# Optimization experiments

Measured on AMD Instinct MI355X. Metric: run time of the kernel, lower is better.

The kernel has to match this reference:

```python
import jax, jax.numpy as jnp
import numpy as np

SUBNET_NUM = 32
BATCH = 131072
H1, H2 = 10, 6          # subnet_arch = [10, 6]
SMOOTH_LAMBDA = 0.001
BN_EPS = 1e-10


def setup_inputs() -> dict:
    key = jax.random.key(0)
    ks = jax.random.split(key, 7)
    f32 = jnp.float32
    x = jax.random.normal(ks[0], (BATCH, SUBNET_NUM), f32)
    # small init scale keeps tanh in its non-saturated (smooth) regime
    W1 = 0.5 * jax.random.normal(ks[1], (SUBNET_NUM, 1, H1), f32)
    b1 = 0.1 * jax.random.normal(ks[2], (SUBNET_NUM, H1), f32)
    W2 = 0.5 * jax.random.normal(ks[3], (SUBNET_NUM, H1, H2), f32)
    b2 = 0.1 * jax.random.normal(ks[4], (SUBNET_NUM, H2), f32)
    W3 = 0.5 * jax.random.normal(ks[5], (SUBNET_NUM, H2, 1), f32)
    b3 = 0.1 * jax.random.normal(ks[6], (SUBNET_NUM, 1), f32)
    return {"x": x, "W1": W1, "b1": b1, "W2": W2, "b2": b2, "W3": W3, "b3": b3}


def _subnet_scalar(x_s, w1, b1, w2, b2, w3, b3):
    """One subnet applied to one scalar input: output and d2out/dx2."""
    def f(xs):
        h = jnp.tanh(xs * w1[0] + b1)        # [H1]  (input dim is 1)
        h = jnp.tanh(h @ w2 + b2)            # [H2]
        return (h @ w3)[0] + b3[0]           # scalar
    out = f(x_s)
    g2 = jax.grad(jax.grad(f))(x_s)          # second derivative wrt the scalar input
    return out, g2


def reference(x, W1, b1, W2, b2, W3, b3):
    # vmap over batch (inner) and over subnets (outer, axis 1 of x / axis 0 of params)
    per_batch = jax.vmap(_subnet_scalar, in_axes=(0, None, None, None, None, None, None))
    per_subnet = jax.vmap(per_batch, in_axes=(1, 0, 0, 0, 0, 0, 0), out_axes=(1, 1))
    out, g2 = per_subnet(x, W1, b1, W2, b2, W3, b3)      # each [BATCH, SUBNET_NUM]

    # BatchNorm (momentum=0.0, center=False, scale=False) in training mode:
    # normalize by batch stats; moving_variance == biased batch variance.
    mean = jnp.mean(out, axis=0)
    var = jnp.mean((out - mean) ** 2, axis=0)
    out_bn = (out - mean) * jax.lax.rsqrt(var + BN_EPS)

    # smooth penalty per subnet: mean(grad2^2) / sqrt(moving_variance)
    penalty = jnp.mean(g2 ** 2, axis=0) / jnp.sqrt(var)
    smooth_loss = SMOOTH_LAMBDA * jnp.sum(penalty)
    return out_bn, smooth_loss
```

## Files before the change

kernel.cpp:

```cpp
#include <hip/hip_runtime.h>

#define BATCH 131072
#define SN 32
#define H1 10
#define H2 6
#define ROWS 128
#define GRID (BATCH / ROWS)
#define TPB 512
#define LDS_STRIDE 33

#define FB 512
#define FT 256

typedef float v2f __attribute__((ext_vector_type(2)));

__device__ __forceinline__ v2f bc(float s) { v2f r; r.x = s; r.y = s; return r; }
__device__ __forceinline__ v2f fma2(v2f a, v2f b, v2f c) {
    return __builtin_elementwise_fma(a, b, c);
}
__device__ __forceinline__ v2f tanh2(v2f x) {
    v2f x2 = x + x;
    v2f e; e.x = __expf(x2.x); e.y = __expf(x2.y);
    v2f e1 = e + bc(1.0f);
    v2f r; r.x = __builtin_amdgcn_rcpf(e1.x); r.y = __builtin_amdgcn_rcpf(e1.y);
    return fma2(bc(-2.0f), r, bc(1.0f));
}

__device__ __forceinline__ float wave_sum(float v) {
    v += __int_as_float(__builtin_amdgcn_update_dpp(
            0, __float_as_int(v), 0x111, 0xf, 0xf, false));
    v += __int_as_float(__builtin_amdgcn_update_dpp(
            0, __float_as_int(v), 0x112, 0xf, 0xf, false));
    v += __int_as_float(__builtin_amdgcn_update_dpp(
            0, __float_as_int(v), 0x114, 0xf, 0xf, false));
    v += __int_as_float(__builtin_amdgcn_update_dpp(
            0, __float_as_int(v), 0x118, 0xf, 0xf, false));
    v += __int_as_float(__builtin_amdgcn_update_dpp(
            0, __float_as_int(v), 0x142, 0xa, 0xf, false));
    v += __int_as_float(__builtin_amdgcn_update_dpp(
            0, __float_as_int(v), 0x143, 0xc, 0xf, false));
    return v;
}

__global__ __launch_bounds__(TPB) void k_main(
    const float* __restrict__ x,
    const float* __restrict__ W1, const float* __restrict__ B1,
    const float* __restrict__ W2, const float* __restrict__ B2,
    const float* __restrict__ W3, const float* __restrict__ B3,
    float* __restrict__ out, float* __restrict__ partial )
{
    __shared__ float xt[ROWS * LDS_STRIDE];
    const int tid = threadIdx.x;
    const int lane = tid & 63;
    const int wave = tid >> 6;
    const int blk = blockIdx.x;

    const float4* xv = (const float4*)(x + (size_t)blk * ROWS * SN);
    #pragma unroll
    for (int it = 0; it < 2; ++it) {
        int v = it * TPB + tid;
        float4 val = xv[v];
        int r = v >> 3;
        int c = (v & 7) << 2;
        float* dst = &xt[r * LDS_STRIDE + c];
        dst[0] = val.x; dst[1] = val.y; dst[2] = val.z; dst[3] = val.w;
    }
    __syncthreads();

    #pragma unroll 1
    for (int si = 0; si < 4; ++si) {
        const int s = __builtin_amdgcn_readfirstlane(si * 8 + wave);
        const float* w1p = W1 + s * H1;
        const float* b1p = B1 + s * H1;
        const float* w2p = W2 + s * H1 * H2;
        const float* b2p = B2 + s * H2;
        const float* w3p = W3 + s * H2;
        const float b3 = B3[s];

        float w1r[H1], b1r[H1];
        #pragma unroll
        for (int i = 0; i < H1; ++i) { w1r[i] = w1p[i]; b1r[i] = b1p[i]; }
        float w2r[H1 * H2];
        #pragma unroll
        for (int k = 0; k < H1 * H2; ++k) w2r[k] = w2p[k];
        float b2r[H2], w3r[H2];
        #pragma unroll
        for (int j = 0; j < H2; ++j) { b2r[j] = b2p[j]; w3r[j] = w3p[j]; }

        v2f xs;
        xs.x = xt[lane * LDS_STRIDE + s];
        xs.y = xt[(lane + 64) * LDS_STRIDE + s];

        v2f t[H1], p[H1], q[H1];
        #pragma unroll
        for (int i = 0; i < H1; ++i) {
            v2f u = fma2(xs, bc(w1r[i]), bc(b1r[i]));
            v2f ti = tanh2(u);
            v2f e = fma2(-ti, ti, bc(1.0f));
            t[i] = ti;
            p[i] = e * bc(w1r[i]);
            q[i] = (ti * p[i]) * bc(w1r[i]);
        }

        v2f o = bc(b3), g2a = bc(0.0f);
        #pragma unroll
        for (int j = 0; j < H2; ++j) {
            v2f vv = bc(b2r[j]), a = bc(0.0f), c = bc(0.0f);
            #pragma unroll
            for (int i = 0; i < H1; ++i) {
                v2f wb = bc(w2r[i * H2 + j]);
                vv = fma2(wb, t[i], vv);
                a  = fma2(wb, p[i], a);
                c  = fma2(wb, q[i], c);
            }
            v2f sj = tanh2(vv);
            v2f dj = fma2(-sj, sj, bc(1.0f));
            v2f aa = a * a;
            v2f h  = fma2(sj, aa, c);
            v2f k  = dj * h;
            o   = fma2(bc(w3r[j]), sj, o);
            g2a = fma2(bc(w3r[j]), k, g2a);
        }

        xt[lane * LDS_STRIDE + s] = o.x;
        xt[(lane + 64) * LDS_STRIDE + s] = o.y;

        v2f s2v = o * o;
        v2f s3v = (g2a * g2a) * bc(4.0f);
        float s1 = wave_sum(o.x + o.y);
        float s2 = wave_sum(s2v.x + s2v.y);
        float s3 = wave_sum(s3v.x + s3v.y);
        if (lane == 63) {
            partial[(size_t)(0 * SN + s) * GRID + blk] = s1;
            partial[(size_t)(1 * SN + s) * GRID + blk] = s2;
            partial[(size_t)(2 * SN + s) * GRID + blk] = s3;
        }
    }
    __syncthreads();

    float4* po = (float4*)out;
    const size_t base = (size_t)blk * (ROWS * SN / 4);
    #pragma unroll
    for (int it = 0; it < 2; ++it) {
        int v = it * TPB + tid;
        int r = v >> 3;
        int c = (v & 7) << 2;
        const float* src = &xt[r * LDS_STRIDE + c];
        float4 w; w.x = src[0]; w.y = src[1]; w.z = src[2]; w.w = src[3];
        po[base + v] = w;
    }
}

__global__ __launch_bounds__(FT) void k_finish(float* __restrict__ out,
                                               const float* __restrict__ partial)
{
    __shared__ double red_s[3 * SN];
    __shared__ float mean_s[SN], inv_s[SN];
    const int tid = threadIdx.x;
    const int lane = tid & 63;
    const int wave = tid >> 6;

    for (int r = wave; r < 3 * SN; r += 4) {
        const float4* pr = (const float4*)(partial + (size_t)r * GRID);
        double sd = 0.0;
        #pragma unroll
        for (int k = 0; k < 4; ++k) {
            float4 v4 = pr[k * 64 + lane];
            sd += (double)v4.x + (double)v4.y + (double)v4.z + (double)v4.w;
        }
        #pragma unroll
        for (int off = 32; off > 0; off >>= 1) sd += __shfl_down(sd, off);
        if (lane == 0) red_s[r] = sd;
    }
    __syncthreads();

    const double invB = 1.0 / (double)BATCH;
    if (tid < SN) {
        double mean = red_s[tid] * invB;
        double var = red_s[SN + tid] * invB - mean * mean;
        if (var < 0.0) var = 0.0;
        mean_s[tid] = (float)mean;
        inv_s[tid] = (float)(1.0 / sqrt(var + 1e-10));
    }
    if (blockIdx.x == 0 && tid == 0) {
        double sum = 0.0;
        for (int s = 0; s < SN; ++s) {
            double mean = red_s[s] * invB;
            double var = red_s[SN + s] * invB - mean * mean;
            if (var < 0.0) var = 0.0;
            sum += (red_s[2 * SN + s] * invB) / sqrt(var);
        }
        out[(size_t)BATCH * SN] = (float)(0.001 * sum);
    }
    __syncthreads();

    float4* p = (float4*)out;
    const int total = BATCH * SN / 4;
    for (int v = blockIdx.x * FT + tid; v < total; v += FB * FT) {
        float4 val = p[v];
        const int c = (v & 7) << 2;
        val.x = (val.x - mean_s[c + 0]) * inv_s[c + 0];
        val.y = (val.y - mean_s[c + 1]) * inv_s[c + 1];
        val.z = (val.z - mean_s[c + 2]) * inv_s[c + 2];
        val.w = (val.w - mean_s[c + 3]) * inv_s[c + 3];
        p[v] = val;
    }
}

extern "C" void kernel_launch(void* const* d_in, const int* in_sizes, int n_in,
                              void* d_out, int out_size, void* d_ws, size_t ws_size,
                              hipStream_t stream) {
    const float* x  = (const float*)d_in[0];
    const float* W1 = (const float*)d_in[1];
    const float* B1 = (const float*)d_in[2];
    const float* W2 = (const float*)d_in[3];
    const float* B2 = (const float*)d_in[4];
    const float* W3 = (const float*)d_in[5];
    const float* B3 = (const float*)d_in[6];

    float* out = (float*)d_out;
    float* partial = (float*)d_ws;

    k_main<<<GRID, TPB, 0, stream>>>(x, W1, B1, W2, B2, W3, B3, out, partial);
    k_finish<<<FB, FT, 0, stream>>>(out, partial);
}
```

Baseline: 132.2 us.

## Move partial-stat reduction into last main block; use exp2-based tanh

The per-block partial sums are now reduced once, by the last block of k_main to finish. That block is detected with an atomic counter plus thread fences and writes double accumulators to the workspace. Before, each of the many k_finish blocks re-read and reduced the whole partial array. k_finish now only reads the final accumulators, computes the penalty with a wave shuffle instead of a serial loop, and runs with more blocks. tanh now uses a scaled exp2 builtin. The counter is reset by block 0 at kernel start, which relies on block 0 running before any other block finishes; that is a small ordering risk.

```diff
diff --git a/kernel.cpp b/kernel.cpp
--- a/kernel.cpp
+++ b/kernel.cpp
@@ -9,7 +9,7 @@
 #define TPB 512
 #define LDS_STRIDE 33
 
-#define FB 512
+#define FB 2048
 #define FT 256
 
 typedef float v2f __attribute__((ext_vector_type(2)));
@@ -18,9 +18,16 @@
 __device__ __forceinline__ v2f fma2(v2f a, v2f b, v2f c) {
     return __builtin_elementwise_fma(a, b, c);
 }
+__device__ __forceinline__ float fexp2(float x) {
+#if __has_builtin(__builtin_amdgcn_exp2f)
+    return __builtin_amdgcn_exp2f(x);
+#else
+    return __expf(0.6931471805599453f * x);
+#endif
+}
 __device__ __forceinline__ v2f tanh2(v2f x) {
-    v2f x2 = x + x;
-    v2f e; e.x = __expf(x2.x); e.y = __expf(x2.y);
+    v2f xl = x * bc(2.885390081777927f);
+    v2f e; e.x = fexp2(xl.x); e.y = fexp2(xl.y);
     v2f e1 = e + bc(1.0f);
     v2f r; r.x = __builtin_amdgcn_rcpf(e1.x); r.y = __builtin_amdgcn_rcpf(e1.y);
     return fma2(bc(-2.0f), r, bc(1.0f));
@@ -47,13 +54,17 @@
     const float* __restrict__ W1, const float* __restrict__ B1,
     const float* __restrict__ W2, const float* __restrict__ B2,
     const float* __restrict__ W3, const float* __restrict__ B3,
-    float* __restrict__ out, float* __restrict__ partial )
+    float* __restrict__ out, float* __restrict__ partial ,
+    double* __restrict__ acc , unsigned* __restrict__ cnt)
 {
     __shared__ float xt[ROWS * LDS_STRIDE];
+    __shared__ unsigned lastflag;
     const int tid = threadIdx.x;
     const int lane = tid & 63;
     const int wave = tid >> 6;
     const int blk = blockIdx.x;
+
+    if (blk == 0 && tid == 0) atomicExch(cnt, 0u);
 
     const float4* xv = (const float4*)(x + (size_t)blk * ROWS * SN);
     #pragma unroll
@@ -149,48 +160,55 @@
         float4 w; w.x = src[0]; w.y = src[1]; w.z = src[2]; w.w = src[3];
         po[base + v] = w;
     }
+
+    __threadfence();
+    if (tid == 0) {
+        unsigned old = atomicAdd(cnt, 1u);
+        lastflag = (old == GRID - 1) ? 1u : 0u;
+    }
+    __syncthreads();
+    if (lastflag) {
+        __threadfence();
+        for (int r = wave; r < 3 * SN; r += 8) {
+            const float4* pr = (const float4*)(partial + (size_t)r * GRID);
+            double sd = 0.0;
+            #pragma unroll
+            for (int k2 = 0; k2 < 4; ++k2) {
+                float4 v4 = pr[k2 * 64 + lane];
+                sd += (double)v4.x + (double)v4.y + (double)v4.z + (double)v4.w;
+            }
+            #pragma unroll
+            for (int off = 32; off > 0; off >>= 1) sd += __shfl_down(sd, off);
+            if (lane == 0) acc[r] = sd;
+        }
+    }
 }
 
 __global__ __launch_bounds__(FT) void k_finish(float* __restrict__ out,
-                                               const float* __restrict__ partial)
+                                               const double* __restrict__ acc)
 {
-    __shared__ double red_s[3 * SN];
     __shared__ float mean_s[SN], inv_s[SN];
     const int tid = threadIdx.x;
-    const int lane = tid & 63;
-    const int wave = tid >> 6;
-
-    for (int r = wave; r < 3 * SN; r += 4) {
-        const float4* pr = (const float4*)(partial + (size_t)r * GRID);
-        double sd = 0.0;
-        #pragma unroll
-        for (int k = 0; k < 4; ++k) {
-            float4 v4 = pr[k * 64 + lane];
-            sd += (double)v4.x + (double)v4.y + (double)v4.z + (double)v4.w;
-        }
-        #pragma unroll
-        for (int off = 32; off > 0; off >>= 1) sd += __shfl_down(sd, off);
-        if (lane == 0) red_s[r] = sd;
-    }
-    __syncthreads();
-
     const double invB = 1.0 / (double)BATCH;
+
     if (tid < SN) {
-        double mean = red_s[tid] * invB;
-        double var = red_s[SN + tid] * invB - mean * mean;
+        double mean = acc[tid] * invB;
+        double var = acc[SN + tid] * invB - mean * mean;
         if (var < 0.0) var = 0.0;
         mean_s[tid] = (float)mean;
         inv_s[tid] = (float)(1.0 / sqrt(var + 1e-10));
     }
-    if (blockIdx.x == 0 && tid == 0) {
-        double sum = 0.0;
-        for (int s = 0; s < SN; ++s) {
-            double mean = red_s[s] * invB;
-            double var = red_s[SN + s] * invB - mean * mean;
+    if (blockIdx.x == 0 && tid < 64) {
+        double term = 0.0;
+        if (tid < SN) {
+            double mean = acc[tid] * invB;
+            double var = acc[SN + tid] * invB - mean * mean;
             if (var < 0.0) var = 0.0;
-            sum += (red_s[2 * SN + s] * invB) / sqrt(var);
-        }
-        out[(size_t)BATCH * SN] = (float)(0.001 * sum);
+            term = (acc[2 * SN + tid] * invB) / sqrt(var);
+        }
+        #pragma unroll
+        for (int off = 16; off > 0; off >>= 1) term += __shfl_down(term, off);
+        if (tid == 0) out[(size_t)BATCH * SN] = (float)(0.001 * term);
     }
     __syncthreads();
 
@@ -220,7 +238,10 @@
 
     float* out = (float*)d_out;
     float* partial = (float*)d_ws;
-
-    k_main<<<GRID, TPB, 0, stream>>>(x, W1, B1, W2, B2, W3, B3, out, partial);
-    k_finish<<<FB, FT, 0, stream>>>(out, partial);
-}
+    double* acc = (double*)((char*)d_ws + (size_t)3 * SN * GRID * sizeof(float));
+    unsigned* cnt = (unsigned*)((char*)acc + 3 * SN * sizeof(double));
+
+    k_main<<<GRID, TPB, 0, stream>>>(x, W1, B1, W2, B2, W3, B3, out, partial,
+                                     acc, cnt);
+    k_finish<<<FB, FT, 0, stream>>>(out, acc);
+}
```

Measured after the change: 300.6 us. +127.3%, slower.
